# Kernel optimization log

Hardware: AMD Instinct MI355X
Metric: run time of the kernel (lower is better)

The kernel has to match this reference:

```python
import jax, jax.numpy as jnp
import numpy as np

B, QL, ML = 8, 128, 1024
QS, KS, H = 512, 512, 256


def setup_inputs() -> dict:
    key = jax.random.key(0)
    ks = jax.random.split(key, 10)
    query = jax.random.normal(ks[0], (B, QL, QS), dtype=jnp.float32)
    memory = jax.random.normal(ks[1], (B, ML, KS), dtype=jnp.float32)
    mask = jax.random.bernoulli(ks[2], 0.1, (B, ML))
    mask = mask.at[:, 0].set(False)  # ensure at least one valid position per row
    s_q = 1.0 / np.sqrt(QS)
    s_k = 1.0 / np.sqrt(KS)
    s_h = 1.0 / np.sqrt(H)
    Wq = jax.random.uniform(ks[3], (H, QS), jnp.float32, -s_q, s_q)
    bq = jax.random.uniform(ks[4], (H,), jnp.float32, -s_q, s_q)
    Wk = jax.random.uniform(ks[5], (H, KS), jnp.float32, -s_k, s_k)
    bk = jax.random.uniform(ks[6], (H,), jnp.float32, -s_k, s_k)
    wl = jax.random.uniform(ks[7], (H,), jnp.float32, -s_h, s_h)
    bl = jax.random.uniform(ks[8], (), jnp.float32, -s_h, s_h)
    return {"query": query, "memory": memory, "mask": mask,
            "Wq": Wq, "bq": bq, "Wk": Wk, "bk": bk, "wl": wl, "bl": bl}


def reference(query, memory, mask, Wq, bq, Wk, bk, wl, bl):
    # q: [B, QL, H], k: [B, ML, H]
    q = jnp.einsum('bqs,hs->bqh', query, Wq) + bq
    k = jnp.einsum('bms,hs->bmh', memory, Wk) + bk
    # additive score: tanh(q + k) projected to scalar  -> [B, QL, ML]
    z = jnp.tanh(q[:, :, None, :] + k[:, None, :, :])  # [B, QL, ML, H]
    logits = jnp.einsum('bqmh,h->bqm', z, wl) + bl
    logits = jnp.where(mask[:, None, :], jnp.float32(-1e18), logits)
    weights = jax.nn.softmax(logits, axis=-1)  # BottleSoftmax over mem_len
    attns = jnp.einsum('bqm,bms->bqs', weights, memory)
    return attns, weights
```

## Files before the change

kernel.cpp:

```cpp
#include <hip/hip_runtime.h>

#define B_  8
#define QL_ 128
#define ML_ 1024
#define KS_ 512
#define H_  256

#define QP_OFF 0
#define KP_OFF 262144
#define MASK_OFF 2359296

__global__ __launch_bounds__(256) void proj_kernel(
    const float* __restrict__ query, const float* __restrict__ memory,
    const float* __restrict__ Wq, const float* __restrict__ bq,
    const float* __restrict__ Wk, const float* __restrict__ bk,
    float* __restrict__ Eq, float* __restrict__ Ek,
    const unsigned char* __restrict__ mraw, unsigned char* __restrict__ mout) {
    const int bid = blockIdx.x;
    const int t = threadIdx.x;

    if (bid == 576) {
        __shared__ int s_not01, s_not0f;
        const unsigned int* w = (const unsigned int*)mraw;
        if (t == 0) { s_not01 = 0; s_not0f = 0; }
        __syncthreads();
        int not01 = 0, not0f = 0;
        for (int i = t; i < 2048; i += 256) {
            unsigned int v = w[i];
            if (v != 0u && v != 1u) not01 = 1;
            if (v != 0u && v != 0x3F800000u) not0f = 1;
        }
        if (not01) atomicOr(&s_not01, 1);
        if (not0f) atomicOr(&s_not0f, 1);
        __syncthreads();
        int wordTyped = (!s_not01) || (!s_not0f);
        for (int i = t; i < B_ * ML_; i += 256) {
            unsigned char mv;
            if (wordTyped) mv = (w[i] != 0u) ? 1 : 0;
            else           mv = mraw[i] ? 1 : 0;
            mout[i] = mv;
        }
        return;
    }

    const float SC = 2.885390081777926815f;
    const int K = 512, N = 256;
    __shared__ float Xs[16][68];
    __shared__ float Ws[16][68];

    const float *X, *W, *bias; float* out; int bm, bn;
    if (bid < 64) { X = query;  W = Wq; bias = bq; out = Eq; bm = bid >> 2;        bn = bid & 3; }
    else          { X = memory; W = Wk; bias = bk; out = Ek; bm = (bid - 64) >> 2; bn = (bid - 64) & 3; }

    const int tx = t & 15, ty = t >> 4;
    const int lr = t >> 2;
    const int lk = (t & 3) << 2;
    const float* Xrow = X + (size_t)(bm * 64 + lr) * K + lk;
    const float* Wrow = W + (size_t)(bn * 64 + lr) * K + lk;
    float acc[4][4] = {};
    float4 xa = *(const float4*)(Xrow);
    float4 wa = *(const float4*)(Wrow);
    for (int k0 = 0; k0 < K; k0 += 16) {
        __syncthreads();
        Xs[lk + 0][lr] = xa.x; Xs[lk + 1][lr] = xa.y;
        Xs[lk + 2][lr] = xa.z; Xs[lk + 3][lr] = xa.w;
        Ws[lk + 0][lr] = wa.x; Ws[lk + 1][lr] = wa.y;
        Ws[lk + 2][lr] = wa.z; Ws[lk + 3][lr] = wa.w;
        __syncthreads();
        if (k0 + 16 < K) {
            xa = *(const float4*)(Xrow + k0 + 16);
            wa = *(const float4*)(Wrow + k0 + 16);
        }
#pragma unroll
        for (int k = 0; k < 16; ++k) {
            float4 av = *(const float4*)(&Xs[k][ty * 4]);
            float4 bv = *(const float4*)(&Ws[k][tx * 4]);
            float a[4] = {av.x, av.y, av.z, av.w};
            float b[4] = {bv.x, bv.y, bv.z, bv.w};
#pragma unroll
            for (int i = 0; i < 4; ++i)
#pragma unroll
                for (int j = 0; j < 4; ++j)
                    acc[i][j] = fmaf(a[i], b[j], acc[i][j]);
        }
    }
    float4 bv = *(const float4*)(bias + bn * 64 + tx * 4);
    float bvec[4] = {bv.x, bv.y, bv.z, bv.w};
#pragma unroll
    for (int i = 0; i < 4; ++i) {
        int m = bm * 64 + ty * 4 + i;
        float4 o;
        o.x = __builtin_amdgcn_exp2f(SC * (acc[i][0] + bvec[0]));
        o.y = __builtin_amdgcn_exp2f(SC * (acc[i][1] + bvec[1]));
        o.z = __builtin_amdgcn_exp2f(SC * (acc[i][2] + bvec[2]));
        o.w = __builtin_amdgcn_exp2f(SC * (acc[i][3] + bvec[3]));
        *(float4*)(out + (size_t)m * N + bn * 64 + tx * 4) = o;
    }
}

__global__ __launch_bounds__(256) void logits_kernel(
    const float* __restrict__ Eq, const float* __restrict__ Ek,
    const float* __restrict__ wl, float* __restrict__ sr) {
    const int bid = blockIdx.x;
    const int b  = bid & 7;
    const int r2 = bid >> 3;
    const int mt = r2 & 7;
    const int qt = r2 >> 3;
    const int tid = threadIdx.x;
    const int m  = tid & 127;
    const int qh = tid >> 7;

    __shared__ float eqs[2048];
    __shared__ float wls[256];
    __shared__ float kq[4][128][4];

    const float* qpb = Eq + ((size_t)(b * QL_ + qt * 8)) * H_;
    const float* kpb = Ek + ((size_t)(b * ML_ + mt * 128)) * H_;

    *(float4*)(&eqs[tid * 4])        = *(const float4*)(qpb + tid * 4);
    *(float4*)(&eqs[1024 + tid * 4]) = *(const float4*)(qpb + 1024 + tid * 4);
    if (tid < 64) *(float4*)(&wls[tid * 4]) = *(const float4*)(wl + tid * 4);

    const int srow = tid & 127;
    const int sq2  = tid >> 7;
    const float* kst = kpb + (size_t)srow * H_ + 8 * sq2;
    float4 a0 = *(const float4*)(kst);
    float4 a1 = *(const float4*)(kst + 4);

    float acc[4] = {0.f, 0.f, 0.f, 0.f};

    for (int c = 0; c < 16; ++c) {
        __syncthreads();
        *(float4*)(&kq[2 * sq2 + 0][srow][0]) = a0;
        *(float4*)(&kq[2 * sq2 + 1][srow][0]) = a1;
        __syncthreads();
        if (c < 15) {
            a0 = *(const float4*)(kst + (c + 1) * 16);
            a1 = *(const float4*)(kst + (c + 1) * 16 + 4);
        }
        const int h0 = c * 16;
#pragma unroll
        for (int quad = 0; quad < 4; ++quad) {
            float4 k4 = *(const float4*)(&kq[quad][m][0]);
            float4 w4 = *(const float4*)(&wls[h0 + quad * 4]);
#pragma unroll
            for (int j2 = 0; j2 < 4; ++j2) {
                float4 q4 = *(const float4*)(&eqs[(qh * 4 + j2) * 256 + h0 + quad * 4]);
                float p0 = fmaf(k4.x, q4.x, 1.0f);
                float p1 = fmaf(k4.y, q4.y, 1.0f);
                float p2 = fmaf(k4.z, q4.z, 1.0f);
                float p3 = fmaf(k4.w, q4.w, 1.0f);
                float p01 = p0 * p1, p23 = p2 * p3;
                float n01 = fmaf(w4.y, p0, w4.x * p1);
                float n23 = fmaf(w4.w, p2, w4.z * p3);
                float Nm  = fmaf(n23, p01, n01 * p23);
                float P   = p01 * p23;
                acc[j2] = fmaf(Nm, __builtin_amdgcn_rcpf(P), acc[j2]);
            }
        }
    }
#pragma unroll
    for (int j2 = 0; j2 < 4; ++j2)
        sr[((size_t)(b * QL_ + qt * 8 + qh * 4 + j2)) * ML_ + mt * 128 + m] = acc[j2];
}

__global__ __launch_bounds__(256) void softmax_kernel(
    float* __restrict__ wrow_io, const unsigned char* __restrict__ mv) {
    const int row = blockIdx.x;
    const int b = row >> 7;
    const int tid = threadIdx.x;
    float* srow = wrow_io + (size_t)row * ML_;
    const unsigned char* mrow = mv + b * ML_;
    __shared__ float red[4];

    float4 s4 = *(const float4*)(srow + tid * 4);
    uchar4 m4 = *(const uchar4*)(mrow + tid * 4);
    float l[4];
    l[0] = m4.x ? -1e18f : -2.0f * s4.x;
    l[1] = m4.y ? -1e18f : -2.0f * s4.y;
    l[2] = m4.z ? -1e18f : -2.0f * s4.z;
    l[3] = m4.w ? -1e18f : -2.0f * s4.w;

    float mx = fmaxf(fmaxf(l[0], l[1]), fmaxf(l[2], l[3]));
#pragma unroll
    for (int off = 32; off >= 1; off >>= 1)
        mx = fmaxf(mx, __shfl_xor(mx, off));
    if ((tid & 63) == 0) red[tid >> 6] = mx;
    __syncthreads();
    mx = fmaxf(fmaxf(red[0], red[1]), fmaxf(red[2], red[3]));
    __syncthreads();

    const float L2E = 1.44269504088896340736f;
    float e[4], s = 0.f;
#pragma unroll
    for (int i = 0; i < 4; ++i) {
        e[i] = __builtin_amdgcn_exp2f((l[i] - mx) * L2E);
        s += e[i];
    }
#pragma unroll
    for (int off = 32; off >= 1; off >>= 1)
        s += __shfl_xor(s, off);
    if ((tid & 63) == 0) red[tid >> 6] = s;
    __syncthreads();
    s = (red[0] + red[1]) + (red[2] + red[3]);
    float inv = __builtin_amdgcn_rcpf(s);
    float4 o = make_float4(e[0] * inv, e[1] * inv, e[2] * inv, e[3] * inv);
    *(float4*)(srow + tid * 4) = o;
}

__global__ __launch_bounds__(256) void attn_out_kernel(
    const float* __restrict__ wgt, const float* __restrict__ mem,
    float* __restrict__ out) {
    const int bid = blockIdx.x;
    const int b  = bid & 7;
    const int j2 = bid >> 3;
    const int mt = j2 & 3;
    const int nt = j2 >> 2;
    const int t = threadIdx.x;
    __shared__ float As[32][34];
    __shared__ float Bs[32][64];

    const int ar = t >> 3, ac = (t & 7) << 2;
    const int br = t >> 4, bc = (t & 15) << 2;
    const float* Ap = wgt + ((size_t)(b * QL_ + mt * 32 + ar)) * ML_ + ac;
    const float* Bp = mem + ((size_t)(b * ML_ + br)) * KS_ + nt * 64 + bc;

    const int tx = t & 15, ty = t >> 4;
    float acc0[4] = {0.f, 0.f, 0.f, 0.f};
    float acc1[4] = {0.f, 0.f, 0.f, 0.f};

    float4 apre = *(const float4*)(Ap);
    float4 bpre0 = *(const float4*)(Bp);
    float4 bpre1 = *(const float4*)(Bp + (size_t)16 * KS_);

    for (int k0 = 0; k0 < ML_; k0 += 32) {
        __syncthreads();
        As[ac + 0][ar] = apre.x; As[ac + 1][ar] = apre.y;
        As[ac + 2][ar] = apre.z; As[ac + 3][ar] = apre.w;
        *(float4*)(&Bs[br][bc])      = bpre0;
        *(float4*)(&Bs[br + 16][bc]) = bpre1;
        __syncthreads();
        if (k0 + 32 < ML_) {
            apre  = *(const float4*)(Ap + k0 + 32);
            bpre0 = *(const float4*)(Bp + (size_t)(k0 + 32) * KS_);
            bpre1 = *(const float4*)(Bp + (size_t)(k0 + 48) * KS_);
        }
#pragma unroll
        for (int kk = 0; kk < 32; ++kk) {
            float2 a2 = *(const float2*)(&As[kk][ty * 2]);
            float4 b4 = *(const float4*)(&Bs[kk][tx * 4]);
            acc0[0] = fmaf(a2.x, b4.x, acc0[0]);
            acc0[1] = fmaf(a2.x, b4.y, acc0[1]);
            acc0[2] = fmaf(a2.x, b4.z, acc0[2]);
            acc0[3] = fmaf(a2.x, b4.w, acc0[3]);
            acc1[0] = fmaf(a2.y, b4.x, acc1[0]);
            acc1[1] = fmaf(a2.y, b4.y, acc1[1]);
            acc1[2] = fmaf(a2.y, b4.z, acc1[2]);
            acc1[3] = fmaf(a2.y, b4.w, acc1[3]);
        }
    }
    size_t orow = ((size_t)(b * QL_ + mt * 32 + ty * 2)) * KS_ + nt * 64 + tx * 4;
    *(float4*)(out + orow)       = make_float4(acc0[0], acc0[1], acc0[2], acc0[3]);
    *(float4*)(out + orow + KS_) = make_float4(acc1[0], acc1[1], acc1[2], acc1[3]);
}

extern "C" void kernel_launch(void* const* d_in, const int* in_sizes, int n_in,
                              void* d_out, int out_size, void* d_ws, size_t ws_size,
                              hipStream_t stream) {
    const float* query  = (const float*)d_in[0];
    const float* memory = (const float*)d_in[1];
    const unsigned char* mask = (const unsigned char*)d_in[2];
    const float* Wq = (const float*)d_in[3];
    const float* bq = (const float*)d_in[4];
    const float* Wk = (const float*)d_in[5];
    const float* bk = (const float*)d_in[6];
    const float* wl = (const float*)d_in[7];

    float* ws = (float*)d_ws;
    float* Eq = ws + QP_OFF;
    float* Ek = ws + KP_OFF;
    unsigned char* mcan = (unsigned char*)(ws + MASK_OFF);

    float* attns = (float*)d_out;
    float* wout  = (float*)d_out + B_ * QL_ * KS_;

    proj_kernel<<<dim3(577), dim3(256), 0, stream>>>(query, memory, Wq, bq, Wk, bk,
                                                     Eq, Ek, mask, mcan);
    logits_kernel<<<dim3(1024), dim3(256), 0, stream>>>(Eq, Ek, wl, wout);
    softmax_kernel<<<dim3(B_ * QL_), dim3(256), 0, stream>>>(wout, mcan);
    attn_out_kernel<<<dim3(256), dim3(256), 0, stream>>>(wout, memory, attns);
}
```

Baseline: 193.7 us.

## Fuse logits with softmax per query pair and double-buffer projection GEMM

The separate logits and softmax kernels become one kernel. Each block computes the full 1024-wide logit row for two queries, keeps it in shared memory, then applies the mask and softmax before writing the weights once. This removes the global write and re-read of the logits and one kernel launch. The projection GEMM gains double-buffered shared-memory tiles with one barrier per k-step and a remapped block index. The cost is that each K tile is now reused by only one query per thread instead of four. That raises shared-memory and L2 traffic per tanh evaluation and halves the block count of the dominant stage.

```diff
diff --git a/kernel.cpp b/kernel.cpp
--- a/kernel.cpp
+++ b/kernel.cpp
@@ -16,10 +16,10 @@
     const float* __restrict__ Wk, const float* __restrict__ bk,
     float* __restrict__ Eq, float* __restrict__ Ek,
     const unsigned char* __restrict__ mraw, unsigned char* __restrict__ mout) {
-    const int bid = blockIdx.x;
+    const int g = blockIdx.x;
     const int t = threadIdx.x;
 
-    if (bid == 576) {
+    if (g == 576) {
         __shared__ int s_not01, s_not0f;
         const unsigned int* w = (const unsigned int*)mraw;
         if (t == 0) { s_not01 = 0; s_not0f = 0; }
@@ -45,36 +45,43 @@
 
     const float SC = 2.885390081777926815f;
     const int K = 512, N = 256;
-    __shared__ float Xs[16][68];
-    __shared__ float Ws[16][68];
-
-    const float *X, *W, *bias; float* out; int bm, bn;
-    if (bid < 64) { X = query;  W = Wq; bias = bq; out = Eq; bm = bid >> 2;        bn = bid & 3; }
-    else          { X = memory; W = Wk; bias = bk; out = Ek; bm = (bid - 64) >> 2; bn = (bid - 64) & 3; }
+    __shared__ float Xs[2][16][68];
+    __shared__ float Ws[2][16][68];
+
+    const int bn = (g & 7) >> 1;
+    const int bm = ((g >> 3) << 1) | (g & 1);
+
+    const float *X, *W, *bias; float* out; int mrow0;
+    if (bm < 16) { X = query;  W = Wq; bias = bq; out = Eq; mrow0 = bm * 64; }
+    else         { X = memory; W = Wk; bias = bk; out = Ek; mrow0 = (bm - 16) * 64; }
 
     const int tx = t & 15, ty = t >> 4;
     const int lr = t >> 2;
     const int lk = (t & 3) << 2;
-    const float* Xrow = X + (size_t)(bm * 64 + lr) * K + lk;
+    const float* Xrow = X + (size_t)(mrow0 + lr) * K + lk;
     const float* Wrow = W + (size_t)(bn * 64 + lr) * K + lk;
+
+    float4 xa[2], wa[2];
+    xa[0] = *(const float4*)(Xrow);       wa[0] = *(const float4*)(Wrow);
+    xa[1] = *(const float4*)(Xrow + 16);  wa[1] = *(const float4*)(Wrow + 16);
+
+    Xs[0][lk + 0][lr] = xa[0].x; Xs[0][lk + 1][lr] = xa[0].y;
+    Xs[0][lk + 2][lr] = xa[0].z; Xs[0][lk + 3][lr] = xa[0].w;
+    Ws[0][lk + 0][lr] = wa[0].x; Ws[0][lk + 1][lr] = wa[0].y;
+    Ws[0][lk + 2][lr] = wa[0].z; Ws[0][lk + 3][lr] = wa[0].w;
+    __syncthreads();
+
     float acc[4][4] = {};
-    float4 xa = *(const float4*)(Xrow);
-    float4 wa = *(const float4*)(Wrow);
-    for (int k0 = 0; k0 < K; k0 += 16) {
-        __syncthreads();
-        Xs[lk + 0][lr] = xa.x; Xs[lk + 1][lr] = xa.y;
-        Xs[lk + 2][lr] = xa.z; Xs[lk + 3][lr] = xa.w;
-        Ws[lk + 0][lr] = wa.x; Ws[lk + 1][lr] = wa.y;
-        Ws[lk + 2][lr] = wa.z; Ws[lk + 3][lr] = wa.w;
-        __syncthreads();
-        if (k0 + 16 < K) {
-            xa = *(const float4*)(Xrow + k0 + 16);
-            wa = *(const float4*)(Wrow + k0 + 16);
+    for (int kt = 0; kt < 32; ++kt) {
+        const int cur = kt & 1;
+        if (kt + 2 < 32) {
+            xa[cur] = *(const float4*)(Xrow + (kt + 2) * 16);
+            wa[cur] = *(const float4*)(Wrow + (kt + 2) * 16);
         }
 #pragma unroll
         for (int k = 0; k < 16; ++k) {
-            float4 av = *(const float4*)(&Xs[k][ty * 4]);
-            float4 bv = *(const float4*)(&Ws[k][tx * 4]);
+            float4 av = *(const float4*)(&Xs[cur][k][ty * 4]);
+            float4 bv = *(const float4*)(&Ws[cur][k][tx * 4]);
             float a[4] = {av.x, av.y, av.z, av.w};
             float b[4] = {bv.x, bv.y, bv.z, bv.w};
 #pragma unroll
@@ -83,12 +90,21 @@
                 for (int j = 0; j < 4; ++j)
                     acc[i][j] = fmaf(a[i], b[j], acc[i][j]);
         }
-    }
+        if (kt + 1 < 32) {
+            const int nxt = cur ^ 1;
+            Xs[nxt][lk + 0][lr] = xa[nxt].x; Xs[nxt][lk + 1][lr] = xa[nxt].y;
+            Xs[nxt][lk + 2][lr] = xa[nxt].z; Xs[nxt][lk + 3][lr] = xa[nxt].w;
+            Ws[nxt][lk + 0][lr] = wa[nxt].x; Ws[nxt][lk + 1][lr] = wa[nxt].y;
+            Ws[nxt][lk + 2][lr] = wa[nxt].z; Ws[nxt][lk + 3][lr] = wa[nxt].w;
+            __syncthreads();
+        }
+    }
+
     float4 bv = *(const float4*)(bias + bn * 64 + tx * 4);
     float bvec[4] = {bv.x, bv.y, bv.z, bv.w};
 #pragma unroll
     for (int i = 0; i < 4; ++i) {
-        int m = bm * 64 + ty * 4 + i;
+        int m = mrow0 + ty * 4 + i;
         float4 o;
         o.x = __builtin_amdgcn_exp2f(SC * (acc[i][0] + bvec[0]));
         o.y = __builtin_amdgcn_exp2f(SC * (acc[i][1] + bvec[1]));
@@ -98,54 +114,58 @@
     }
 }
 
-__global__ __launch_bounds__(256) void logits_kernel(
+__global__ __launch_bounds__(256) void logits_sm_kernel(
     const float* __restrict__ Eq, const float* __restrict__ Ek,
-    const float* __restrict__ wl, float* __restrict__ sr) {
+    const float* __restrict__ wl, const unsigned char* __restrict__ mcan,
+    float* __restrict__ wout) {
     const int bid = blockIdx.x;
-    const int b  = bid & 7;
-    const int r2 = bid >> 3;
-    const int mt = r2 & 7;
-    const int qt = r2 >> 3;
+    const int b   = bid & 7;
+    const int q0  = (bid >> 3) * 2;
     const int tid = threadIdx.x;
-    const int m  = tid & 127;
-    const int qh = tid >> 7;
-
-    __shared__ float eqs[2048];
+    const int qi   = tid >> 7;
+    const int mloc = tid & 127;
+
+    __shared__ float eqs[2][256];
     __shared__ float wls[256];
     __shared__ float kq[4][128][4];
-
-    const float* qpb = Eq + ((size_t)(b * QL_ + qt * 8)) * H_;
-    const float* kpb = Ek + ((size_t)(b * ML_ + mt * 128)) * H_;
-
-    *(float4*)(&eqs[tid * 4])        = *(const float4*)(qpb + tid * 4);
-    *(float4*)(&eqs[1024 + tid * 4]) = *(const float4*)(qpb + 1024 + tid * 4);
-    if (tid < 64) *(float4*)(&wls[tid * 4]) = *(const float4*)(wl + tid * 4);
-
+    __shared__ float accs[8][256];
+    __shared__ unsigned int msksw[256];
+    __shared__ float redm[4];
+
+    if (tid < 128)
+        *(float4*)(&eqs[tid >> 6][(tid & 63) * 4]) =
+            *(const float4*)(Eq + ((size_t)(b * QL_ + q0 + (tid >> 6))) * H_ + (tid & 63) * 4);
+    else if (tid < 192)
+        *(float4*)(&wls[(tid - 128) * 4]) = *(const float4*)(wl + (tid - 128) * 4);
+    msksw[tid] = ((const unsigned int*)(mcan + b * ML_))[tid];
+
+    const float* kbase = Ek + (size_t)(b * ML_) * H_;
     const int srow = tid & 127;
     const int sq2  = tid >> 7;
-    const float* kst = kpb + (size_t)srow * H_ + 8 * sq2;
-    float4 a0 = *(const float4*)(kst);
-    float4 a1 = *(const float4*)(kst + 4);
-
-    float acc[4] = {0.f, 0.f, 0.f, 0.f};
-
-    for (int c = 0; c < 16; ++c) {
-        __syncthreads();
-        *(float4*)(&kq[2 * sq2 + 0][srow][0]) = a0;
-        *(float4*)(&kq[2 * sq2 + 1][srow][0]) = a1;
-        __syncthreads();
-        if (c < 15) {
-            a0 = *(const float4*)(kst + (c + 1) * 16);
-            a1 = *(const float4*)(kst + (c + 1) * 16 + 4);
-        }
-        const int h0 = c * 16;
-#pragma unroll
-        for (int quad = 0; quad < 4; ++quad) {
-            float4 k4 = *(const float4*)(&kq[quad][m][0]);
-            float4 w4 = *(const float4*)(&wls[h0 + quad * 4]);
-#pragma unroll
-            for (int j2 = 0; j2 < 4; ++j2) {
-                float4 q4 = *(const float4*)(&eqs[(qh * 4 + j2) * 256 + h0 + quad * 4]);
+
+    float4 a0 = *(const float4*)(kbase + (size_t)srow * H_ + 8 * sq2);
+    float4 a1 = *(const float4*)(kbase + (size_t)srow * H_ + 8 * sq2 + 4);
+
+    for (int mt = 0; mt < 8; ++mt) {
+        float acc = 0.f;
+        for (int c = 0; c < 16; ++c) {
+            __syncthreads();
+            *(float4*)(&kq[2 * sq2 + 0][srow][0]) = a0;
+            *(float4*)(&kq[2 * sq2 + 1][srow][0]) = a1;
+            __syncthreads();
+            int s1 = mt * 16 + c + 1;
+            if (s1 < 128) {
+                int pm = s1 >> 4, pc = s1 & 15;
+                const float* ka = kbase + (size_t)(pm * 128 + srow) * H_ + pc * 16 + 8 * sq2;
+                a0 = *(const float4*)(ka);
+                a1 = *(const float4*)(ka + 4);
+            }
+            const int h0 = c * 16;
+#pragma unroll
+            for (int quad = 0; quad < 4; ++quad) {
+                float4 k4 = *(const float4*)(&kq[quad][mloc][0]);
+                float4 w4 = *(const float4*)(&wls[h0 + quad * 4]);
+                float4 q4 = *(const float4*)(&eqs[qi][h0 + quad * 4]);
                 float p0 = fmaf(k4.x, q4.x, 1.0f);
                 float p1 = fmaf(k4.y, q4.y, 1.0f);
                 float p2 = fmaf(k4.z, q4.z, 1.0f);
@@ -155,57 +175,53 @@
                 float n23 = fmaf(w4.w, p2, w4.z * p3);
                 float Nm  = fmaf(n23, p01, n01 * p23);
                 float P   = p01 * p23;
-                acc[j2] = fmaf(Nm, __builtin_amdgcn_rcpf(P), acc[j2]);
+                acc = fmaf(Nm, __builtin_amdgcn_rcpf(P), acc);
             }
         }
-    }
-#pragma unroll
-    for (int j2 = 0; j2 < 4; ++j2)
-        sr[((size_t)(b * QL_ + qt * 8 + qh * 4 + j2)) * ML_ + mt * 128 + m] = acc[j2];
-}
-
-__global__ __launch_bounds__(256) void softmax_kernel(
-    float* __restrict__ wrow_io, const unsigned char* __restrict__ mv) {
-    const int row = blockIdx.x;
-    const int b = row >> 7;
-    const int tid = threadIdx.x;
-    float* srow = wrow_io + (size_t)row * ML_;
-    const unsigned char* mrow = mv + b * ML_;
-    __shared__ float red[4];
-
-    float4 s4 = *(const float4*)(srow + tid * 4);
-    uchar4 m4 = *(const uchar4*)(mrow + tid * 4);
-    float l[4];
-    l[0] = m4.x ? -1e18f : -2.0f * s4.x;
-    l[1] = m4.y ? -1e18f : -2.0f * s4.y;
-    l[2] = m4.z ? -1e18f : -2.0f * s4.z;
-    l[3] = m4.w ? -1e18f : -2.0f * s4.w;
-
-    float mx = fmaxf(fmaxf(l[0], l[1]), fmaxf(l[2], l[3]));
+        accs[mt][tid] = acc;
+    }
+    __syncthreads();
+
+    const unsigned char* mrow = (const unsigned char*)msksw;
+    float l[8];
+    unsigned int mbits = 0;
+    float mx = -3.0e38f;
+#pragma unroll
+    for (int mt = 0; mt < 8; ++mt) {
+        float v = accs[mt][tid];
+        int mk = mrow[mt * 128 + mloc];
+        mbits |= (unsigned)(mk != 0) << mt;
+        l[mt] = mk ? -3.0e38f : (-2.0f * v);
+        mx = fmaxf(mx, l[mt]);
+    }
 #pragma unroll
     for (int off = 32; off >= 1; off >>= 1)
         mx = fmaxf(mx, __shfl_xor(mx, off));
-    if ((tid & 63) == 0) red[tid >> 6] = mx;
-    __syncthreads();
-    mx = fmaxf(fmaxf(red[0], red[1]), fmaxf(red[2], red[3]));
+    if ((tid & 63) == 0) redm[tid >> 6] = mx;
+    __syncthreads();
+    mx = fmaxf(redm[qi * 2], redm[qi * 2 + 1]);
     __syncthreads();
 
     const float L2E = 1.44269504088896340736f;
-    float e[4], s = 0.f;
-#pragma unroll
-    for (int i = 0; i < 4; ++i) {
-        e[i] = __builtin_amdgcn_exp2f((l[i] - mx) * L2E);
-        s += e[i];
+    float e[8], s = 0.f;
+#pragma unroll
+    for (int mt = 0; mt < 8; ++mt) {
+        e[mt] = ((mbits >> mt) & 1) ? 0.f
+                : __builtin_amdgcn_exp2f((l[mt] - mx) * L2E);
+        s += e[mt];
     }
 #pragma unroll
     for (int off = 32; off >= 1; off >>= 1)
         s += __shfl_xor(s, off);
-    if ((tid & 63) == 0) red[tid >> 6] = s;
-    __syncthreads();
-    s = (red[0] + red[1]) + (red[2] + red[3]);
+    if ((tid & 63) == 0) redm[tid >> 6] = s;
+    __syncthreads();
+    s = redm[qi * 2] + redm[qi * 2 + 1];
     float inv = __builtin_amdgcn_rcpf(s);
-    float4 o = make_float4(e[0] * inv, e[1] * inv, e[2] * inv, e[3] * inv);
-    *(float4*)(srow + tid * 4) = o;
+
+    float* wrow = wout + ((size_t)(b * QL_ + q0 + qi)) * ML_;
+#pragma unroll
+    for (int mt = 0; mt < 8; ++mt)
+        wrow[mt * 128 + mloc] = e[mt] * inv;
 }
 
 __global__ __launch_bounds__(256) void attn_out_kernel(
@@ -286,7 +302,6 @@
 
     proj_kernel<<<dim3(577), dim3(256), 0, stream>>>(query, memory, Wq, bq, Wk, bk,
                                                      Eq, Ek, mask, mcan);
-    logits_kernel<<<dim3(1024), dim3(256), 0, stream>>>(Eq, Ek, wl, wout);
-    softmax_kernel<<<dim3(B_ * QL_), dim3(256), 0, stream>>>(wout, mcan);
+    logits_sm_kernel<<<dim3(512), dim3(256), 0, stream>>>(Eq, Ek, wl, mcan, wout);
     attn_out_kernel<<<dim3(256), dim3(256), 0, stream>>>(wout, memory, attns);
 }
```

Result: slower. 241.1 us (+24.5%).

## Fuse softmax into logits with deferred normalization; double-buffer projection and logits tiles

Applied to the files above, without the earlier changes.

Drops the separate max-subtracting softmax pass. The logits kernel now writes unnormalized exp weights, zero where masked, plus per-tile partial row sums. The attention-output GEMM scales its result by the reciprocal row sum, and a light kernel normalizes the stored weights afterwards. The projection and logits kernels also move to double-buffered shared memory with a K-tile of 32 and one barrier per step, and the projection grid is remapped. The risk is that skipping the max subtraction relies on the logits being bounded, which tanh and the small wl make likely, so overflow is unlikely.

```diff
diff --git a/kernel.cpp b/kernel.cpp
--- a/kernel.cpp
+++ b/kernel.cpp
@@ -9,6 +9,7 @@
 #define QP_OFF 0
 #define KP_OFF 262144
 #define MASK_OFF 2359296
+#define PSUM_OFF 2361344
 
 __global__ __launch_bounds__(256) void proj_kernel(
     const float* __restrict__ query, const float* __restrict__ memory,
@@ -16,10 +17,10 @@
     const float* __restrict__ Wk, const float* __restrict__ bk,
     float* __restrict__ Eq, float* __restrict__ Ek,
     const unsigned char* __restrict__ mraw, unsigned char* __restrict__ mout) {
-    const int bid = blockIdx.x;
+    const int g = blockIdx.x;
     const int t = threadIdx.x;
 
-    if (bid == 576) {
+    if (g == 576) {
         __shared__ int s_not01, s_not0f;
         const unsigned int* w = (const unsigned int*)mraw;
         if (t == 0) { s_not01 = 0; s_not0f = 0; }
@@ -45,36 +46,52 @@
 
     const float SC = 2.885390081777926815f;
     const int K = 512, N = 256;
-    __shared__ float Xs[16][68];
-    __shared__ float Ws[16][68];
-
-    const float *X, *W, *bias; float* out; int bm, bn;
-    if (bid < 64) { X = query;  W = Wq; bias = bq; out = Eq; bm = bid >> 2;        bn = bid & 3; }
-    else          { X = memory; W = Wk; bias = bk; out = Ek; bm = (bid - 64) >> 2; bn = (bid - 64) & 3; }
+    __shared__ float Xs[2][32][68];
+    __shared__ float Ws[2][32][68];
+
+    const int bn = (g & 7) >> 1;
+    const int bm = ((g >> 3) << 1) | (g & 1);
+
+    const float *X, *W, *bias; float* out; int mrow0;
+    if (bm < 16) { X = query;  W = Wq; bias = bq; out = Eq; mrow0 = bm * 64; }
+    else         { X = memory; W = Wk; bias = bk; out = Ek; mrow0 = (bm - 16) * 64; }
 
     const int tx = t & 15, ty = t >> 4;
     const int lr = t >> 2;
     const int lk = (t & 3) << 2;
-    const float* Xrow = X + (size_t)(bm * 64 + lr) * K + lk;
+    const float* Xrow = X + (size_t)(mrow0 + lr) * K + lk;
     const float* Wrow = W + (size_t)(bn * 64 + lr) * K + lk;
+
+    float4 xsl[2][2], wsl[2][2];
+    xsl[0][0] = *(const float4*)(Xrow);      xsl[0][1] = *(const float4*)(Xrow + 16);
+    wsl[0][0] = *(const float4*)(Wrow);      wsl[0][1] = *(const float4*)(Wrow + 16);
+    xsl[1][0] = *(const float4*)(Xrow + 32); xsl[1][1] = *(const float4*)(Xrow + 48);
+    wsl[1][0] = *(const float4*)(Wrow + 32); wsl[1][1] = *(const float4*)(Wrow + 48);
+
+    Xs[0][lk + 0][lr] = xsl[0][0].x; Xs[0][lk + 1][lr] = xsl[0][0].y;
+    Xs[0][lk + 2][lr] = xsl[0][0].z; Xs[0][lk + 3][lr] = xsl[0][0].w;
+    Xs[0][lk + 16][lr] = xsl[0][1].x; Xs[0][lk + 17][lr] = xsl[0][1].y;
+    Xs[0][lk + 18][lr] = xsl[0][1].z; Xs[0][lk + 19][lr] = xsl[0][1].w;
+    Ws[0][lk + 0][lr] = wsl[0][0].x; Ws[0][lk + 1][lr] = wsl[0][0].y;
+    Ws[0][lk + 2][lr] = wsl[0][0].z; Ws[0][lk + 3][lr] = wsl[0][0].w;
+    Ws[0][lk + 16][lr] = wsl[0][1].x; Ws[0][lk + 17][lr] = wsl[0][1].y;
+    Ws[0][lk + 18][lr] = wsl[0][1].z; Ws[0][lk + 19][lr] = wsl[0][1].w;
+    __syncthreads();
+
     float acc[4][4] = {};
-    float4 xa = *(const float4*)(Xrow);
-    float4 wa = *(const float4*)(Wrow);
-    for (int k0 = 0; k0 < K; k0 += 16) {
-        __syncthreads();
-        Xs[lk + 0][lr] = xa.x; Xs[lk + 1][lr] = xa.y;
-        Xs[lk + 2][lr] = xa.z; Xs[lk + 3][lr] = xa.w;
-        Ws[lk + 0][lr] = wa.x; Ws[lk + 1][lr] = wa.y;
-        Ws[lk + 2][lr] = wa.z; Ws[lk + 3][lr] = wa.w;
-        __syncthreads();
-        if (k0 + 16 < K) {
-            xa = *(const float4*)(Xrow + k0 + 16);
-            wa = *(const float4*)(Wrow + k0 + 16);
-        }
-#pragma unroll
-        for (int k = 0; k < 16; ++k) {
-            float4 av = *(const float4*)(&Xs[k][ty * 4]);
-            float4 bv = *(const float4*)(&Ws[k][tx * 4]);
+    for (int kt = 0; kt < 16; ++kt) {
+        const int cur = kt & 1;
+        if (kt + 2 < 16) {
+            const int o = (kt + 2) * 32;
+            xsl[cur][0] = *(const float4*)(Xrow + o);
+            xsl[cur][1] = *(const float4*)(Xrow + o + 16);
+            wsl[cur][0] = *(const float4*)(Wrow + o);
+            wsl[cur][1] = *(const float4*)(Wrow + o + 16);
+        }
+#pragma unroll
+        for (int k = 0; k < 32; ++k) {
+            float4 av = *(const float4*)(&Xs[cur][k][ty * 4]);
+            float4 bv = *(const float4*)(&Ws[cur][k][tx * 4]);
             float a[4] = {av.x, av.y, av.z, av.w};
             float b[4] = {bv.x, bv.y, bv.z, bv.w};
 #pragma unroll
@@ -83,12 +100,25 @@
                 for (int j = 0; j < 4; ++j)
                     acc[i][j] = fmaf(a[i], b[j], acc[i][j]);
         }
-    }
+        if (kt + 1 < 16) {
+            const int nxt = cur ^ 1;
+            Xs[nxt][lk + 0][lr] = xsl[nxt][0].x; Xs[nxt][lk + 1][lr] = xsl[nxt][0].y;
+            Xs[nxt][lk + 2][lr] = xsl[nxt][0].z; Xs[nxt][lk + 3][lr] = xsl[nxt][0].w;
+            Xs[nxt][lk + 16][lr] = xsl[nxt][1].x; Xs[nxt][lk + 17][lr] = xsl[nxt][1].y;
+            Xs[nxt][lk + 18][lr] = xsl[nxt][1].z; Xs[nxt][lk + 19][lr] = xsl[nxt][1].w;
+            Ws[nxt][lk + 0][lr] = wsl[nxt][0].x; Ws[nxt][lk + 1][lr] = wsl[nxt][0].y;
+            Ws[nxt][lk + 2][lr] = wsl[nxt][0].z; Ws[nxt][lk + 3][lr] = wsl[nxt][0].w;
+            Ws[nxt][lk + 16][lr] = wsl[nxt][1].x; Ws[nxt][lk + 17][lr] = wsl[nxt][1].y;
+            Ws[nxt][lk + 18][lr] = wsl[nxt][1].z; Ws[nxt][lk + 19][lr] = wsl[nxt][1].w;
+            __syncthreads();
+        }
+    }
+
     float4 bv = *(const float4*)(bias + bn * 64 + tx * 4);
     float bvec[4] = {bv.x, bv.y, bv.z, bv.w};
 #pragma unroll
     for (int i = 0; i < 4; ++i) {
-        int m = bm * 64 + ty * 4 + i;
+        int m = mrow0 + ty * 4 + i;
         float4 o;
         o.x = __builtin_amdgcn_exp2f(SC * (acc[i][0] + bvec[0]));
         o.y = __builtin_amdgcn_exp2f(SC * (acc[i][1] + bvec[1]));
@@ -100,7 +130,8 @@
 
 __global__ __launch_bounds__(256) void logits_kernel(
     const float* __restrict__ Eq, const float* __restrict__ Ek,
-    const float* __restrict__ wl, float* __restrict__ sr) {
+    const float* __restrict__ wl, const unsigned char* __restrict__ mcan,
+    float* __restrict__ wout, float* __restrict__ psum) {
     const int bid = blockIdx.x;
     const int b  = bid & 7;
     const int r2 = bid >> 3;
@@ -112,7 +143,8 @@
 
     __shared__ float eqs[2048];
     __shared__ float wls[256];
-    __shared__ float kq[4][128][4];
+    __shared__ float kq[2][4][128][4];
+    __shared__ float sred[4][4];
 
     const float* qpb = Eq + ((size_t)(b * QL_ + qt * 8)) * H_;
     const float* kpb = Ek + ((size_t)(b * ML_ + mt * 128)) * H_;
@@ -121,27 +153,25 @@
     *(float4*)(&eqs[1024 + tid * 4]) = *(const float4*)(qpb + 1024 + tid * 4);
     if (tid < 64) *(float4*)(&wls[tid * 4]) = *(const float4*)(wl + tid * 4);
 
-    const int srow = tid & 127;
-    const int sq2  = tid >> 7;
-    const float* kst = kpb + (size_t)srow * H_ + 8 * sq2;
+    const float* kst = kpb + (size_t)m * H_ + 8 * qh;
     float4 a0 = *(const float4*)(kst);
     float4 a1 = *(const float4*)(kst + 4);
+    *(float4*)(&kq[0][2 * qh + 0][m][0]) = a0;
+    *(float4*)(&kq[0][2 * qh + 1][m][0]) = a1;
+    __syncthreads();
 
     float acc[4] = {0.f, 0.f, 0.f, 0.f};
 
     for (int c = 0; c < 16; ++c) {
-        __syncthreads();
-        *(float4*)(&kq[2 * sq2 + 0][srow][0]) = a0;
-        *(float4*)(&kq[2 * sq2 + 1][srow][0]) = a1;
-        __syncthreads();
         if (c < 15) {
             a0 = *(const float4*)(kst + (c + 1) * 16);
             a1 = *(const float4*)(kst + (c + 1) * 16 + 4);
         }
+        const int buf = c & 1;
         const int h0 = c * 16;
 #pragma unroll
         for (int quad = 0; quad < 4; ++quad) {
-            float4 k4 = *(const float4*)(&kq[quad][m][0]);
+            float4 k4 = *(const float4*)(&kq[buf][quad][m][0]);
             float4 w4 = *(const float4*)(&wls[h0 + quad * 4]);
 #pragma unroll
             for (int j2 = 0; j2 < 4; ++j2) {
@@ -158,59 +188,45 @@
                 acc[j2] = fmaf(Nm, __builtin_amdgcn_rcpf(P), acc[j2]);
             }
         }
-    }
-#pragma unroll
-    for (int j2 = 0; j2 < 4; ++j2)
-        sr[((size_t)(b * QL_ + qt * 8 + qh * 4 + j2)) * ML_ + mt * 128 + m] = acc[j2];
-}
-
-__global__ __launch_bounds__(256) void softmax_kernel(
-    float* __restrict__ wrow_io, const unsigned char* __restrict__ mv) {
-    const int row = blockIdx.x;
-    const int b = row >> 7;
-    const int tid = threadIdx.x;
-    float* srow = wrow_io + (size_t)row * ML_;
-    const unsigned char* mrow = mv + b * ML_;
-    __shared__ float red[4];
-
-    float4 s4 = *(const float4*)(srow + tid * 4);
-    uchar4 m4 = *(const uchar4*)(mrow + tid * 4);
-    float l[4];
-    l[0] = m4.x ? -1e18f : -2.0f * s4.x;
-    l[1] = m4.y ? -1e18f : -2.0f * s4.y;
-    l[2] = m4.z ? -1e18f : -2.0f * s4.z;
-    l[3] = m4.w ? -1e18f : -2.0f * s4.w;
-
-    float mx = fmaxf(fmaxf(l[0], l[1]), fmaxf(l[2], l[3]));
-#pragma unroll
-    for (int off = 32; off >= 1; off >>= 1)
-        mx = fmaxf(mx, __shfl_xor(mx, off));
-    if ((tid & 63) == 0) red[tid >> 6] = mx;
+        if (c < 15) {
+            *(float4*)(&kq[buf ^ 1][2 * qh + 0][m][0]) = a0;
+            *(float4*)(&kq[buf ^ 1][2 * qh + 1][m][0]) = a1;
+            __syncthreads();
+        }
+    }
+
+    const float N2L = -2.885390081777926815f;
+    const int mk = mcan[b * ML_ + mt * 128 + m];
+    float u[4];
+#pragma unroll
+    for (int j2 = 0; j2 < 4; ++j2) {
+        u[j2] = mk ? 0.f : __builtin_amdgcn_exp2f(N2L * acc[j2]);
+        wout[((size_t)(b * QL_ + qt * 8 + qh * 4 + j2)) * ML_ + mt * 128 + m] = u[j2];
+    }
+
+    float r[4] = {u[0], u[1], u[2], u[3]};
+#pragma unroll
+    for (int off = 32; off >= 1; off >>= 1) {
+#pragma unroll
+        for (int j2 = 0; j2 < 4; ++j2)
+            r[j2] += __shfl_xor(r[j2], off);
+    }
+    if ((tid & 63) == 0) {
+#pragma unroll
+        for (int j2 = 0; j2 < 4; ++j2)
+            sred[tid >> 6][j2] = r[j2];
+    }
     __syncthreads();
-    mx = fmaxf(fmaxf(red[0], red[1]), fmaxf(red[2], red[3]));
-    __syncthreads();
-
-    const float L2E = 1.44269504088896340736f;
-    float e[4], s = 0.f;
-#pragma unroll
-    for (int i = 0; i < 4; ++i) {
-        e[i] = __builtin_amdgcn_exp2f((l[i] - mx) * L2E);
-        s += e[i];
-    }
-#pragma unroll
-    for (int off = 32; off >= 1; off >>= 1)
-        s += __shfl_xor(s, off);
-    if ((tid & 63) == 0) red[tid >> 6] = s;
-    __syncthreads();
-    s = (red[0] + red[1]) + (red[2] + red[3]);
-    float inv = __builtin_amdgcn_rcpf(s);
-    float4 o = make_float4(e[0] * inv, e[1] * inv, e[2] * inv, e[3] * inv);
-    *(float4*)(srow + tid * 4) = o;
+    if (tid < 8) {
+        const int q = tid;
+        float v = sred[(q >> 2) * 2][q & 3] + sred[(q >> 2) * 2 + 1][q & 3];
+        psum[((size_t)(b * QL_ + qt * 8 + q)) * 8 + mt] = v;
+    }
 }
 
 __global__ __launch_bounds__(256) void attn_out_kernel(
     const float* __restrict__ wgt, const float* __restrict__ mem,
-    float* __restrict__ out) {
+    const float* __restrict__ psum, float* __restrict__ out) {
     const int bid = blockIdx.x;
     const int b  = bid & 7;
     const int j2 = bid >> 3;
@@ -259,9 +275,31 @@
             acc1[3] = fmaf(a2.y, b4.w, acc1[3]);
         }
     }
+    const float* ps = psum + ((size_t)(b * QL_ + mt * 32 + ty * 2)) * 8;
+    float rs0 = 0.f, rs1 = 0.f;
+#pragma unroll
+    for (int i = 0; i < 8; ++i) { rs0 += ps[i]; rs1 += ps[8 + i]; }
+    float inv0 = __builtin_amdgcn_rcpf(rs0);
+    float inv1 = __builtin_amdgcn_rcpf(rs1);
+
     size_t orow = ((size_t)(b * QL_ + mt * 32 + ty * 2)) * KS_ + nt * 64 + tx * 4;
-    *(float4*)(out + orow)       = make_float4(acc0[0], acc0[1], acc0[2], acc0[3]);
-    *(float4*)(out + orow + KS_) = make_float4(acc1[0], acc1[1], acc1[2], acc1[3]);
+    *(float4*)(out + orow)       = make_float4(acc0[0] * inv0, acc0[1] * inv0,
+                                               acc0[2] * inv0, acc0[3] * inv0);
+    *(float4*)(out + orow + KS_) = make_float4(acc1[0] * inv1, acc1[1] * inv1,
+                                               acc1[2] * inv1, acc1[3] * inv1);
+}
+
+__global__ __launch_bounds__(256) void scale_weights(
+    float* __restrict__ wout, const float* __restrict__ psum) {
+    const int row = blockIdx.x;
+    const int tid = threadIdx.x;
+    const float* ps = psum + (size_t)row * 8;
+    float rs = ((ps[0] + ps[1]) + (ps[2] + ps[3])) +
+               ((ps[4] + ps[5]) + (ps[6] + ps[7]));
+    float inv = __builtin_amdgcn_rcpf(rs);
+    float4* p = (float4*)(wout + (size_t)row * ML_ + tid * 4);
+    float4 v = *p;
+    *p = make_float4(v.x * inv, v.y * inv, v.z * inv, v.w * inv);
 }
 
 extern "C" void kernel_launch(void* const* d_in, const int* in_sizes, int n_in,
@@ -280,13 +318,14 @@
     float* Eq = ws + QP_OFF;
     float* Ek = ws + KP_OFF;
     unsigned char* mcan = (unsigned char*)(ws + MASK_OFF);
+    float* psum = ws + PSUM_OFF;
 
     float* attns = (float*)d_out;
     float* wout  = (float*)d_out + B_ * QL_ * KS_;
 
     proj_kernel<<<dim3(577), dim3(256), 0, stream>>>(query, memory, Wq, bq, Wk, bk,
                                                      Eq, Ek, mask, mcan);
-    logits_kernel<<<dim3(1024), dim3(256), 0, stream>>>(Eq, Ek, wl, wout);
-    softmax_kernel<<<dim3(B_ * QL_), dim3(256), 0, stream>>>(wout, mcan);
-    attn_out_kernel<<<dim3(256), dim3(256), 0, stream>>>(wout, memory, attns);
-}
+    logits_kernel<<<dim3(1024), dim3(256), 0, stream>>>(Eq, Ek, wl, mcan, wout, psum);
+    attn_out_kernel<<<dim3(256), dim3(256), 0, stream>>>(wout, memory, psum, attns);
+    scale_weights<<<dim3(B_ * QL_), dim3(256), 0, stream>>>(wout, psum);
+}
```

After: 234.7 us. 1.21x slower.
